# Kernel optimization log

Hardware: AMD Instinct MI355X
Metric: run time of the kernel (lower is better)

The kernel has to match this reference:

```python
import jax, jax.numpy as jnp
import numpy as np

B, C, N, D, K, M, E, G = 2, 64, 16384, 3, 128, 1, 262144, 3


def setup_inputs() -> dict:
    key = jax.random.key(0)
    ks = jax.random.split(key, 15)
    scale = 1.0 / (C * C)
    return {
        "x": jax.random.normal(ks[0], (B, C, N), jnp.float32),
        "nodes": jax.random.uniform(ks[1], (B, N, D), jnp.float32),
        "node_weights": jax.random.uniform(ks[2], (B, N, M), jnp.float32),
        "geo": jax.random.normal(ks[3], (B, G, N), jnp.float32),
        "directed_edges": jax.random.randint(ks[4], (B, E, 2), 0, N, jnp.int32),
        "edge_gradient_weights": 0.1 * jax.random.normal(ks[5], (B, E, D), jnp.float32),
        "modes": jax.random.normal(ks[6], (K, D, M), jnp.float32),
        "weights_c": scale * jax.random.uniform(ks[7], (C, C, K, M), jnp.float32),
        "weights_s": scale * jax.random.uniform(ks[8], (C, C, K, M), jnp.float32),
        "weights_0": scale * jax.random.uniform(ks[9], (C, C, 1, M), jnp.float32),
        "W": jax.random.normal(ks[10], (C, C), jnp.float32) / np.sqrt(C),
        "gw": jax.random.normal(ks[11], (C, C * D), jnp.float32) / np.sqrt(C * D),
        "geo_wx": jax.random.normal(ks[12], (C, G), jnp.float32) / np.sqrt(G),
        "wx": jax.random.normal(ks[13], (C, C), jnp.float32) / np.sqrt(C),
        "w2": jax.random.normal(ks[14], (C, C), jnp.float32) / np.sqrt(C),
    }


def reference(x, nodes, node_weights, geo, directed_edges, edge_gradient_weights,
              modes, weights_c, weights_s, weights_0, W, gw, geo_wx, wx, w2):
    # ---- Fourier bases: cos(kx), sin(kx), 1 -------------------------------
    temp = jnp.einsum('bxd,kdw->bxkw', nodes, modes)          # [B,N,K,M]
    bases_c, bases_s = jnp.cos(temp), jnp.sin(temp)
    b, n = temp.shape[0], temp.shape[1]
    bases_0 = jnp.ones((b, n, 1, temp.shape[3]), temp.dtype)
    nw = node_weights[:, :, None, :]                          # quadrature weights
    wb_c, wb_s, wb_0 = bases_c * nw, bases_s * nw, bases_0 * nw

    # ---- Spectral convolution (non-uniform Fourier neural layer) ----------
    x_c = jnp.einsum('bix,bxkw->bikw', x, wb_c)
    x_s = -jnp.einsum('bix,bxkw->bikw', x, wb_s)
    x_0 = jnp.einsum('bix,bxkw->bikw', x, wb_0)
    f_c = jnp.einsum('bikw,iokw->bokw', x_c, weights_c) - jnp.einsum('bikw,iokw->bokw', x_s, weights_s)
    f_s = jnp.einsum('bikw,iokw->bokw', x_s, weights_c) + jnp.einsum('bikw,iokw->bokw', x_c, weights_s)
    f_0 = jnp.einsum('bikw,iokw->bokw', x_0, weights_0)
    x1 = (jnp.einsum('bokw,bxkw->box', f_0, bases_0)
          + 2.0 * jnp.einsum('bokw,bxkw->box', f_c, bases_c)
          - 2.0 * jnp.einsum('bokw,bxkw->box', f_s, bases_s))

    # ---- Pointwise linear W ----------------------------------------------
    x2 = jnp.einsum('oi,bix->box', W, x)

    # ---- Least-squares gradient via edge gather + scatter-add -------------
    fT = jnp.transpose(x, (0, 2, 1))                          # [B,N,C]
    tgt, src = directed_edges[..., 0], directed_edges[..., 1]  # [B,E]
    f_src = jnp.take_along_axis(fT, src[:, :, None], axis=1)   # [B,E,C]
    f_tgt = jnp.take_along_axis(fT, tgt[:, :, None], axis=1)
    df = f_src - f_tgt
    # message[b,e,c,d] = w[b,e,d] * df[b,e,c], flattened c-major -> [B,E,C*D]
    msg = (df[..., :, None] * edge_gradient_weights[..., None, :]).reshape(b, tgt.shape[1], -1)
    gradf = jnp.zeros((b, n, msg.shape[-1]), msg.dtype).at[jnp.arange(b)[:, None], tgt].add(msg)
    x3 = jnp.einsum('og,bng->bon', gw, gradf)                  # [B,C,N]

    # ---- Geo embedding: w2 @ (softsign(geo_wx@geo) * (wx@x)) --------------
    h = jax.nn.soft_sign(jnp.einsum('og,bgx->box', geo_wx, geo)) * jnp.einsum('oi,bix->box', wx, x)
    x4 = jnp.einsum('oi,bix->box', w2, h)

    return jax.nn.gelu(x1 + x2 + x3 + x4, approximate=False)
```

## Files before the change

### kernel.cpp

```cpp
#include <hip/hip_runtime.h>
#include <hip/hip_fp16.h>
#include <math.h>

#define BB 2
#define CC 64
#define NN 16384
#define DD 3
#define KK 128
#define EE 262144
#define GG 3
#define PP 128
#define LL (NN/PP)
#define KTOT 576

typedef short bf16x8 __attribute__((ext_vector_type(8)));
typedef float f32x4  __attribute__((ext_vector_type(4)));

__device__ __forceinline__ short f2bf(float f) {
    unsigned u = __float_as_uint(f);
    u += 0x7FFF + ((u >> 16) & 1);
    return (short)(u >> 16);
}
__device__ __forceinline__ float bf2f(unsigned short u) {
    return __uint_as_float(((unsigned)u) << 16);
}

constexpr size_t OFF_XB   = 0;
constexpr size_t OFF_PC   = OFF_XB   + (size_t)BB*NN*32;
constexpr size_t OFF_PS   = OFF_PC   + (size_t)BB*PP*CC*KK;
constexpr size_t OFF_BIN4 = OFF_PC;
constexpr size_t OFF_AC   = OFF_PS   + (size_t)BB*PP*CC*KK;
constexpr size_t OFF_AS   = OFF_AC   + (size_t)BB*CC*KK;
constexpr size_t OFF_F0   = OFF_AS   + (size_t)BB*CC*KK;
constexpr size_t OFF_X0   = OFF_F0   + (size_t)BB*CC;
constexpr size_t OFF_CNT  = OFF_X0   + (size_t)BB*CC;
constexpr size_t OFF_OFFS = OFF_CNT  + (size_t)BB*NN;
constexpr size_t OFF_RANK = OFF_OFFS + (size_t)BB*NN;
constexpr size_t OFF_GRB  = OFF_RANK + (size_t)BB*EE;
constexpr size_t OFF_APAN = OFF_GRB  + (size_t)BB*NN*96;
constexpr size_t OFF_GWXT = OFF_APAN + (size_t)BB*KTOT*CC/2;

#define S_A0 (BB*(NN/64))
#define S_A1 (S_A0 + BB*CC)
#define S_A2 (S_A1 + (BB*EE)/256)
#define S_A3 (S_A2 + 48)
#define S_A4 (S_A3 + BB*PP*4)
__global__ void __launch_bounds__(256) k1(const float* __restrict__ x,
                                          const float* __restrict__ nwt,
                                          const int* __restrict__ edges,
                                          const float* __restrict__ W,
                                          const float* __restrict__ gw,
                                          const float* __restrict__ geo_wx,
                                          const float* __restrict__ w2,
                                          const float* __restrict__ nodes,
                                          const float* __restrict__ modes,
                                          unsigned short* __restrict__ xB,
                                          float* __restrict__ x0,
                                          int* __restrict__ counts,
                                          int* __restrict__ rank,
                                          float* __restrict__ gwxT,
                                          short* __restrict__ ApanB,
                                          float* __restrict__ pc,
                                          float* __restrict__ ps) {
    int blk = blockIdx.x;
    int tid = threadIdx.x;
    __shared__ __align__(16) char smem[36864];
    if (blk < S_A0) {
        float (*tile)[65] = (float (*)[65])smem;
        int b = blk / (NN/64);
        int n0 = (blk % (NN/64)) * 64;
        int c = tid & 63, r4 = tid >> 6;
        for (int rr = 0; rr < 16; rr++) {
            int i = r4*16 + rr;
            tile[i][c] = x[((size_t)b*CC + i)*NN + n0 + c];
        }
        __syncthreads();
        for (int rr = 0; rr < 16; rr++) {
            int nn = r4*16 + rr;
            xB[((size_t)b*NN + n0 + nn)*64 + c] = (unsigned short)f2bf(tile[c][nn]);
        }
    } else if (blk < S_A1) {
        float* red = (float*)smem;
        int bi = blk - S_A0;
        int b = bi >> 6, i = bi & 63;
        const float4* __restrict__ xr = (const float4*)&x[((size_t)b*CC + i)*NN];
        const float4* __restrict__ wr = (const float4*)&nwt[(size_t)b*NN];
        float s = 0.f;
        for (int t = tid; t < NN/4; t += 256) {
            float4 xv = xr[t];
            float4 wv = wr[t];
            s += xv.x*wv.x + xv.y*wv.y + xv.z*wv.z + xv.w*wv.w;
        }
        red[tid] = s;
        __syncthreads();
        for (int off = 128; off > 0; off >>= 1) {
            if (tid < off) red[tid] += red[tid+off];
            __syncthreads();
        }
        if (tid == 0) x0[b*CC + i] = red[0];
    } else if (blk < S_A2) {
        int idx = (blk - S_A1)*256 + tid;
        int tgt = edges[(size_t)idx*2 + 0];
        int b = idx / EE;
        rank[idx] = atomicAdd(&counts[b*NN + tgt], 1);
    } else if (blk < S_A3) {
        int idx = (blk - S_A2)*256 + tid;
        if (idx < CC*CC) {
            int j = idx>>6, o = idx&63;
            short wv  = f2bf(W[o*CC+j]);
            short w2v = f2bf(w2[o*CC+j]);
            ApanB[((size_t)(0*CC+o))*KTOT + 256 + j] = wv;
            ApanB[((size_t)(1*CC+o))*KTOT + 256 + j] = wv;
            ApanB[((size_t)(0*CC+o))*KTOT + 320 + j] = w2v;
            ApanB[((size_t)(1*CC+o))*KTOT + 320 + j] = w2v;
        }
        if (idx < CC*CC*DD) {
            int g = idx>>6, o = idx&63;
            short gv = f2bf(gw[o*(CC*DD)+g]);
            ApanB[((size_t)(0*CC+o))*KTOT + 384 + g] = gv;
            ApanB[((size_t)(1*CC+o))*KTOT + 384 + g] = gv;
        }
        if (idx < GG*CC) { int g = idx>>6, i = idx&63; gwxT[idx] = geo_wx[i*GG+g]; }
    } else {
        short* Axw = (short*)smem;
        short* Bc  = (short*)(smem + 17408);
        short* Bsn = (short*)(smem + 17408 + 8704);
        float* ndl = (float*)(smem + 17408 + 8704 + 8704);
        int bc = blk - S_A3;
        int b = bc >> 9;
        int rem = bc & 511;
        int chunk = rem >> 2;
        int kt = rem & 3;
        int k0 = kt * 32;
        int nbase = chunk * LL;
        int lane = tid & 63;
        int w = tid >> 6;
        int col = lane & 15;
        int quad = lane >> 4;
        int wk = w & 1;
        int wi = w >> 1;

        for (int e = tid; e < LL*3; e += 256) ndl[e] = nodes[((size_t)b*NN + nbase)*3 + e];
#pragma unroll
        for (int s = 0; s < 8; s++) {
            int e = tid + s*256;
            int i = e >> 5, seg = e & 31;
            float4 xv = *(const float4*)&x[((size_t)b*CC + i)*NN + nbase + seg*4];
            float4 wv = *(const float4*)&nwt[(size_t)b*NN + nbase + seg*4];
            unsigned lo = (unsigned)(unsigned short)f2bf(xv.x*wv.x)
                        | ((unsigned)(unsigned short)f2bf(xv.y*wv.y) << 16);
            unsigned hi = (unsigned)(unsigned short)f2bf(xv.z*wv.z)
                        | ((unsigned)(unsigned short)f2bf(xv.w*wv.w) << 16);
            *(uint2*)&Axw[i*136 + seg*4] = make_uint2(lo, hi);
        }
        __syncthreads();
#pragma unroll
        for (int s = 0; s < 16; s++) {
            int e = tid + s*256;
            int n = e & 127, kl = e >> 7;
            int k = k0 + kl;
            float t = ndl[n*3+0]*modes[k*3+0] + ndl[n*3+1]*modes[k*3+1]
                    + ndl[n*3+2]*modes[k*3+2];
            Bc [kl*136 + n] = f2bf(__cosf(t));
            Bsn[kl*136 + n] = f2bf(__sinf(t));
        }
        __syncthreads();

        f32x4 ac[2], as4[2];
#pragma unroll
        for (int it = 0; it < 2; it++)
#pragma unroll
            for (int r = 0; r < 4; r++) { ac[it][r] = 0.f; as4[it][r] = 0.f; }

        int rowB = (wk*16 + col)*136;
#pragma unroll
        for (int ns = 0; ns < 4; ns++) {
            int koff = ns*32 + quad*8;
            bf16x8 bcf = *(bf16x8*)&Bc [rowB + koff];
            bf16x8 bsf = *(bf16x8*)&Bsn[rowB + koff];
#pragma unroll
            for (int it = 0; it < 2; it++) {
                int itile = wi*2 + it;
                bf16x8 af = *(bf16x8*)&Axw[(itile*16 + col)*136 + koff];
                ac[it]  = __builtin_amdgcn_mfma_f32_16x16x32_bf16(af, bcf, ac[it], 0, 0, 0);
                as4[it] = __builtin_amdgcn_mfma_f32_16x16x32_bf16(af, bsf, as4[it], 0, 0, 0);
            }
        }
        int base = (b*PP + chunk)*CC;
        int kw = k0 + wk*16 + col;
#pragma unroll
        for (int it = 0; it < 2; it++) {
#pragma unroll
            for (int r = 0; r < 4; r++) {
                int i = (wi*2 + it)*16 + quad*4 + r;
                pc[(size_t)(base + i)*KK + kw] = ac[it][r];
                ps[(size_t)(base + i)*KK + kw] = as4[it][r];
            }
        }
    }
}

__global__ void __launch_bounds__(256) k2(const float* __restrict__ pc, const float* __restrict__ ps,
                                          float* __restrict__ Ac, float* __restrict__ As,
                                          const int* __restrict__ counts,
                                          int* __restrict__ offsets) {
    int blk = blockIdx.x;
    int tid = threadIdx.x;
    if (blk < 256) {
        int idx = blk*64 + (tid >> 2);
        int sub = tid & 3;
        if (idx >= BB*CC*KK) return;
        int b = idx / (CC*KK);
        int r = idx % (CC*KK);
        float sc = 0.f, ss = 0.f;
        for (int ch = sub; ch < PP; ch += 4) {
            size_t o = ((size_t)(b*PP + ch)*CC)*KK + r;
            sc += pc[o]; ss += ps[o];
        }
        sc += __shfl_xor(sc, 1); sc += __shfl_xor(sc, 2);
        ss += __shfl_xor(ss, 1); ss += __shfl_xor(ss, 2);
        if (sub == 0) { Ac[idx] = sc; As[idx] = ss; }
    } else {
        int b = blk - 256;
        __shared__ int part[256];
        int base = b*NN + tid*64;
        int s = 0;
        for (int j = 0; j < 64; j++) s += counts[base + j];
        part[tid] = s;
        __syncthreads();
        for (int off = 1; off < 256; off <<= 1) {
            int v = (tid >= off) ? part[tid - off] : 0;
            __syncthreads();
            part[tid] += v;
            __syncthreads();
        }
        int excl = part[tid] - s;
        for (int j = 0; j < 64; j++) {
            int c = counts[base + j];
            offsets[base + j] = excl;
            excl += c;
        }
    }
}

__global__ void __launch_bounds__(256) k3(const float* __restrict__ Ac, const float* __restrict__ As_,
                                          const float* __restrict__ wc, const float* __restrict__ wsw,
                                          const float* __restrict__ w0, const float* __restrict__ x0,
                                          const int* __restrict__ edges, const float* __restrict__ egw,
                                          const int* __restrict__ offs, const int* __restrict__ rank,
                                          float4* __restrict__ bin4,
                                          short* __restrict__ ApanB, float* __restrict__ f0) {
    int idx = blockIdx.x;
    int tid = threadIdx.x;
    if (idx >= BB*CC*2) {
        int e = (idx - BB*CC*2)*256 + tid;
        int b = e / EE;
        int tgt = edges[(size_t)e*2+0];
        int src = edges[(size_t)e*2+1];
        const float* __restrict__ ew = &egw[(size_t)e*3];
        float e0 = ew[0], e1 = ew[1], e2 = ew[2];
        int pos = offs[b*NN+tgt] + rank[e];
        bin4[(size_t)b*EE + pos] = make_float4(__int_as_float(src), e0, e1, e2);
        return;
    }
    int b = idx / (CC*2);
    int rem = idx % (CC*2);
    int o = rem >> 1, khalf = rem & 1;
    int kl = tid & 63, ig = tid >> 6;
    int k = khalf*64 + kl;
    float fc = 0.f, fs = 0.f;
    for (int ii = 0; ii < 16; ii++) {
        int i = ig*16 + ii;
        float a_c = Ac[(b*CC+i)*KK + k];
        float a_s = As_[(b*CC+i)*KK + k];
        float wcc = wc[((size_t)(i*CC+o))*KK + k];
        float wss = wsw[((size_t)(i*CC+o))*KK + k];
        fc += a_c*wcc + a_s*wss;
        fs += a_c*wss - a_s*wcc;
    }
    __shared__ float rc[256], rs[256];
    __shared__ float f0s[64];
    rc[tid] = fc; rs[tid] = fs;
    if (khalf == 0 && tid < 64) f0s[tid] = x0[b*CC + tid] * w0[tid*CC + o];
    __syncthreads();
    if (ig == 0) {
        fc = rc[kl] + rc[64+kl] + rc[128+kl] + rc[192+kl];
        fs = rs[kl] + rs[64+kl] + rs[128+kl] + rs[192+kl];
        unsigned pk = (unsigned)(unsigned short)f2bf(2.f*fc)
                    | ((unsigned)(unsigned short)f2bf(-2.f*fs) << 16);
        ((unsigned*)ApanB)[((size_t)(b*CC + o))*(KTOT/2) + k] = pk;
    }
    if (khalf == 0 && tid == 0) {
        float acc = 0.f;
        for (int i = 0; i < 64; i++) acc += f0s[i];
        f0[b*CC+o] = acc;
    }
}

#define ECAP 1024
__global__ void __launch_bounds__(256) k_edge(const unsigned short* __restrict__ xB,
                                              const int* __restrict__ offsets,
                                              const float4* __restrict__ bin4,
                                              unsigned short* __restrict__ gradfB) {
    int blk = blockIdx.x;
    int b = blk / (NN/16);
    int n0 = (blk % (NN/16)) * 16;
    int tid = threadIdx.x;
    int lane = tid & 63;
    int w = tid >> 6;
    __shared__ float4 ebuf[ECAP];
    __shared__ float gl[16][193];
    __shared__ int soff[17];
    if (tid < 16) soff[tid] = offsets[b*NN + n0 + tid];
    if (tid == 16) soff[16] = (n0 + 16 < NN) ? offsets[b*NN + n0 + 16] : EE;
    __syncthreads();
    int base = soff[0];
    int end  = soff[16];
    const unsigned short* __restrict__ xBb = xB + (size_t)b*NN*64 + lane;

    float a0[4], a1[4], a2[4], s0[4], s1[4], s2[4];
#pragma unroll
    for (int q = 0; q < 4; q++) { a0[q]=a1[q]=a2[q]=0.f; s0[q]=s1[q]=s2[q]=0.f; }

    for (int cs = base; cs < end; cs += ECAP) {
        int ce = min(cs + ECAP, end);
        __syncthreads();
        for (int t = cs + tid; t < ce; t += 256)
            ebuf[t - cs] = bin4[(size_t)b*EE + t];
        __syncthreads();
#pragma unroll
        for (int q = 0; q < 4; q++) {
            int nl = w*4 + q;
            int js = max(soff[nl], cs);
            int je = min(soff[nl+1], ce);
#pragma unroll 4
            for (int j = js; j < je; j++) {
                float4 e = ebuf[j - cs];
                int src = __float_as_int(e.x);
                float xs = bf2f(xBb[(size_t)src*64]);
                a0[q] = fmaf(xs, e.y, a0[q]);
                a1[q] = fmaf(xs, e.z, a1[q]);
                a2[q] = fmaf(xs, e.w, a2[q]);
                s0[q] += e.y; s1[q] += e.z; s2[q] += e.w;
            }
        }
    }
    __syncthreads();
#pragma unroll
    for (int q = 0; q < 4; q++) {
        int nl = w*4 + q;
        float xtgt = bf2f(xBb[(size_t)(n0 + nl)*64]);
        gl[nl][lane*3+0] = a0[q] - xtgt*s0[q];
        gl[nl][lane*3+1] = a1[q] - xtgt*s1[q];
        gl[nl][lane*3+2] = a2[q] - xtgt*s2[q];
    }
    __syncthreads();
    for (int t = tid; t < 16*192; t += 256) {
        int nl = t / 192, g = t % 192;
        gradfB[((size_t)(b*NN + n0 + nl))*192 + g] = (unsigned short)f2bf(gl[nl][g]);
    }
}

__global__ void __launch_bounds__(256) k_gemm(const unsigned short* __restrict__ xB,
                                              const float* __restrict__ nodes,
                                              const float* __restrict__ modes,
                                              const float* __restrict__ geo,
                                              const unsigned short* __restrict__ gradfB,
                                              const short* __restrict__ ApanB,
                                              const float* __restrict__ f0,
                                              const float* __restrict__ wx,
                                              const float* __restrict__ gwxT,
                                              float* __restrict__ out) {
    int blk = blockIdx.x;
    int b  = blk >> 8;
    int n0 = (blk & 255) * 64;
    int tid = threadIdx.x;
    int lane = tid & 63;
    int w = tid >> 6;
    int w16 = w * 16;
    int col  = lane & 15;
    int quad = lane >> 4;
    int quad8 = quad * 8;
    int quad4 = quad * 4;

    __shared__ __align__(16) short As[64*72];
    __shared__ __align__(16) short Bs[64*72];
    __shared__ __align__(16) short Ws[64*72];
    __shared__ float ndl[192];
    __shared__ float geo3[192];

    for (int e = tid; e < 4096; e += 256) {
        int i = e >> 6, j = e & 63;
        Ws[i*72 + j] = f2bf(wx[i*64 + j]);
    }
    if (tid < 192) ndl[tid]  = nodes[((size_t)b*NN + n0)*3 + tid];
    if (tid < 192) geo3[tid] = geo[((size_t)b*GG + (tid >> 6))*NN + n0 + (tid & 63)];

    f32x4 acc[4], xwa[4];
    float f0v[4];
#pragma unroll
    for (int r = 0; r < 4; r++) f0v[r] = f0[b*CC + w16 + quad4 + r];
#pragma unroll
    for (int nt = 0; nt < 4; nt++) {
#pragma unroll
        for (int r = 0; r < 4; r++) { acc[nt][r] = f0v[r]; xwa[nt][r] = 0.f; }
    }

    const short* __restrict__ Ab = ApanB + ((size_t)b*CC)*KTOT;

    for (int c = 0; c < 9; c++) {
        __syncthreads();
        for (int e = tid; e < 512; e += 256) {
            int o = e >> 3, seg = e & 7;
            *(uint4*)&As[o*72 + seg*8] =
                *(const uint4*)&Ab[(size_t)o*KTOT + c*64 + seg*8];
        }
        if (c < 4) {
#pragma unroll
            for (int s = 0; s < 8; s++) {
                int e = tid + s*256;
                int n = e >> 5, kpl = e & 31;
                int kp = c*32 + kpl;
                float t = ndl[n*3+0]*modes[kp*3+0] + ndl[n*3+1]*modes[kp*3+1]
                        + ndl[n*3+2]*modes[kp*3+2];
                unsigned pk = (unsigned)(unsigned short)f2bf(__cosf(t))
                            | ((unsigned)(unsigned short)f2bf(__sinf(t)) << 16);
                ((unsigned*)Bs)[n*36 + kpl] = pk;
            }
        } else if (c == 4) {
            for (int e = tid; e < 512; e += 256) {
                int n = e >> 3, seg = e & 7;
                *(uint4*)&Bs[n*72 + seg*8] =
                    *(const uint4*)&xB[((size_t)(b*NN + n0 + n))*64 + seg*8];
            }
        } else if (c == 5) {
#pragma unroll
            for (int r = 0; r < 4; r++) {
                int i = w16 + quad4 + r;
                float g0 = gwxT[i], g1 = gwxT[64+i], g2 = gwxT[128+i];
#pragma unroll
                for (int nt = 0; nt < 4; nt++) {
                    int n = nt*16 + col;
                    float t = g0*geo3[n] + g1*geo3[64+n] + g2*geo3[128+n];
                    float ssv = t / (1.f + fabsf(t));
                    Bs[n*72 + i] = f2bf(ssv * xwa[nt][r]);
                }
            }
        } else {
            const unsigned short* __restrict__ src = gradfB + (size_t)(c-6)*64;
            for (int e = tid; e < 512; e += 256) {
                int n = e >> 3, seg = e & 7;
                *(uint4*)&Bs[n*72 + seg*8] =
                    *(const uint4*)&src[((size_t)(b*NN + n0 + n))*192 + seg*8];
            }
        }
        __syncthreads();
        int rowA = (w16 + col) * 72;
#pragma unroll
        for (int ko = 0; ko < 2; ko++) {
            int koff = ko*32 + quad8;
            bf16x8 af = *(bf16x8*)&As[rowA + koff];
            if (c == 4) {
                bf16x8 wf = *(bf16x8*)&Ws[rowA + koff];
#pragma unroll
                for (int nt = 0; nt < 4; nt++) {
                    bf16x8 bfv = *(bf16x8*)&Bs[(nt*16 + col)*72 + koff];
                    acc[nt] = __builtin_amdgcn_mfma_f32_16x16x32_bf16(af, bfv, acc[nt], 0, 0, 0);
                    xwa[nt] = __builtin_amdgcn_mfma_f32_16x16x32_bf16(wf, bfv, xwa[nt], 0, 0, 0);
                }
            } else {
#pragma unroll
                for (int nt = 0; nt < 4; nt++) {
                    bf16x8 bfv = *(bf16x8*)&Bs[(nt*16 + col)*72 + koff];
                    acc[nt] = __builtin_amdgcn_mfma_f32_16x16x32_bf16(af, bfv, acc[nt], 0, 0, 0);
                }
            }
        }
    }
#pragma unroll
    for (int nt = 0; nt < 4; nt++) {
#pragma unroll
        for (int r = 0; r < 4; r++) {
            int o = w16 + quad4 + r;
            float v = acc[nt][r];
            float g = 0.5f * v * (1.f + erff(v * 0.70710678118654752f));
            out[((size_t)b*CC + o)*NN + n0 + nt*16 + col] = g;
        }
    }
}

extern "C" void kernel_launch(void* const* d_in, const int* in_sizes, int n_in,
                              void* d_out, int out_size, void* d_ws, size_t ws_size,
                              hipStream_t stream) {
    const float* x      = (const float*)d_in[0];
    const float* nodes  = (const float*)d_in[1];
    const float* nwt    = (const float*)d_in[2];
    const float* geo    = (const float*)d_in[3];
    const int*   edges  = (const int*)d_in[4];
    const float* egw    = (const float*)d_in[5];
    const float* modes  = (const float*)d_in[6];
    const float* wc     = (const float*)d_in[7];
    const float* wsw    = (const float*)d_in[8];
    const float* w0     = (const float*)d_in[9];
    const float* W      = (const float*)d_in[10];
    const float* gw     = (const float*)d_in[11];
    const float* geo_wx = (const float*)d_in[12];
    const float* wx     = (const float*)d_in[13];
    const float* w2     = (const float*)d_in[14];

    float* ws   = (float*)d_ws;
    unsigned short* xB  = (unsigned short*)(ws + OFF_XB);
    float* pc   = ws + OFF_PC;
    float* ps   = ws + OFF_PS;
    float* Ac   = ws + OFF_AC;
    float* As_  = ws + OFF_AS;
    float* f0   = ws + OFF_F0;
    float* x0   = ws + OFF_X0;
    int*  counts = (int*)(ws + OFF_CNT);
    int*  offs   = (int*)(ws + OFF_OFFS);
    int*  rank   = (int*)(ws + OFF_RANK);
    float4* bin4 = (float4*)(ws + OFF_BIN4);
    unsigned short* gradfB = (unsigned short*)(ws + OFF_GRB);
    short* ApanB  = (short*)(ws + OFF_APAN);
    float* gwxT   = ws + OFF_GWXT;
    float* out  = (float*)d_out;

    hipMemsetAsync(counts, 0, (size_t)(BB*NN)*sizeof(int), stream);

    k1 <<<S_A4, 256, 0, stream>>>(x, nwt, edges, W, gw, geo_wx, w2, nodes, modes,
                                  xB, x0, counts, rank, gwxT, ApanB, pc, ps);
    k2 <<<256 + BB, 256, 0, stream>>>(pc, ps, Ac, As_, counts, offs);
    k3 <<<BB*CC*2 + (BB*EE)/256, 256, 0, stream>>>(Ac, As_, wc, wsw, w0, x0,
                                                   edges, egw, offs, rank, bin4, ApanB, f0);
    k_edge <<<BB*(NN/16), 256, 0, stream>>>(xB, offs, bin4, gradfB);
    k_gemm <<<BB*(NN/64), 256, 0, stream>>>(xB, nodes, modes, geo, gradfB, ApanB, f0,
                                            wx, gwxT, out);
}
```

Before: 198.3 us.

## Fuse edge-gradient gather into GEMM kernel, keeping gradf in shared memory

Merges the edge gather/accumulate kernel into the GEMM/epilogue kernel. Each 64-node block now computes its own gradient features in four 16-node passes and writes them as bf16 into shared memory, where the GEMM consumes them directly. This removes the global gradfB round-trip and one kernel launch. In exchange, the fused kernel uses about 56 KB of shared memory and launches 512 blocks instead of 2048, which lowers occupancy and parallelism in the latency-bound gather phase.

Result: slower. 208.3 us (+5.1%).

```diff
diff --git a/kernel.cpp b/kernel.cpp
--- a/kernel.cpp
+++ b/kernel.cpp
@@ -297,80 +297,18 @@
     }
 }
 
-#define ECAP 1024
-__global__ void __launch_bounds__(256) k_edge(const unsigned short* __restrict__ xB,
-                                              const int* __restrict__ offsets,
-                                              const float4* __restrict__ bin4,
-                                              unsigned short* __restrict__ gradfB) {
-    int blk = blockIdx.x;
-    int b = blk / (NN/16);
-    int n0 = (blk % (NN/16)) * 16;
-    int tid = threadIdx.x;
-    int lane = tid & 63;
-    int w = tid >> 6;
-    __shared__ float4 ebuf[ECAP];
-    __shared__ float gl[16][193];
-    __shared__ int soff[17];
-    if (tid < 16) soff[tid] = offsets[b*NN + n0 + tid];
-    if (tid == 16) soff[16] = (n0 + 16 < NN) ? offsets[b*NN + n0 + 16] : EE;
-    __syncthreads();
-    int base = soff[0];
-    int end  = soff[16];
-    const unsigned short* __restrict__ xBb = xB + (size_t)b*NN*64 + lane;
-
-    float a0[4], a1[4], a2[4], s0[4], s1[4], s2[4];
-#pragma unroll
-    for (int q = 0; q < 4; q++) { a0[q]=a1[q]=a2[q]=0.f; s0[q]=s1[q]=s2[q]=0.f; }
-
-    for (int cs = base; cs < end; cs += ECAP) {
-        int ce = min(cs + ECAP, end);
-        __syncthreads();
-        for (int t = cs + tid; t < ce; t += 256)
-            ebuf[t - cs] = bin4[(size_t)b*EE + t];
-        __syncthreads();
-#pragma unroll
-        for (int q = 0; q < 4; q++) {
-            int nl = w*4 + q;
-            int js = max(soff[nl], cs);
-            int je = min(soff[nl+1], ce);
-#pragma unroll 4
-            for (int j = js; j < je; j++) {
-                float4 e = ebuf[j - cs];
-                int src = __float_as_int(e.x);
-                float xs = bf2f(xBb[(size_t)src*64]);
-                a0[q] = fmaf(xs, e.y, a0[q]);
-                a1[q] = fmaf(xs, e.z, a1[q]);
-                a2[q] = fmaf(xs, e.w, a2[q]);
-                s0[q] += e.y; s1[q] += e.z; s2[q] += e.w;
-            }
-        }
-    }
-    __syncthreads();
-#pragma unroll
-    for (int q = 0; q < 4; q++) {
-        int nl = w*4 + q;
-        float xtgt = bf2f(xBb[(size_t)(n0 + nl)*64]);
-        gl[nl][lane*3+0] = a0[q] - xtgt*s0[q];
-        gl[nl][lane*3+1] = a1[q] - xtgt*s1[q];
-        gl[nl][lane*3+2] = a2[q] - xtgt*s2[q];
-    }
-    __syncthreads();
-    for (int t = tid; t < 16*192; t += 256) {
-        int nl = t / 192, g = t % 192;
-        gradfB[((size_t)(b*NN + n0 + nl))*192 + g] = (unsigned short)f2bf(gl[nl][g]);
-    }
-}
-
-__global__ void __launch_bounds__(256) k_gemm(const unsigned short* __restrict__ xB,
-                                              const float* __restrict__ nodes,
-                                              const float* __restrict__ modes,
-                                              const float* __restrict__ geo,
-                                              const unsigned short* __restrict__ gradfB,
-                                              const short* __restrict__ ApanB,
-                                              const float* __restrict__ f0,
-                                              const float* __restrict__ wx,
-                                              const float* __restrict__ gwxT,
-                                              float* __restrict__ out) {
+#define ECAP2 512
+__global__ void __launch_bounds__(256) k_eg(const unsigned short* __restrict__ xB,
+                                            const int* __restrict__ offsets,
+                                            const float4* __restrict__ bin4,
+                                            const float* __restrict__ nodes,
+                                            const float* __restrict__ modes,
+                                            const float* __restrict__ geo,
+                                            const short* __restrict__ ApanB,
+                                            const float* __restrict__ f0,
+                                            const float* __restrict__ wx,
+                                            const float* __restrict__ gwxT,
+                                            float* __restrict__ out) {
     int blk = blockIdx.x;
     int b  = blk >> 8;
     int n0 = (blk & 255) * 64;
@@ -383,19 +321,73 @@
     int quad8 = quad * 8;
     int quad4 = quad * 4;
 
-    __shared__ __align__(16) short As[64*72];
-    __shared__ __align__(16) short Bs[64*72];
-    __shared__ __align__(16) short Ws[64*72];
-    __shared__ float ndl[192];
-    __shared__ float geo3[192];
+    __shared__ __align__(16) char smem[56832];
+    short* As = (short*)smem;
+    short* Bs = (short*)(smem + 9216);
+    short* Ws = (short*)(smem + 18432);
+    float4* ebuf = (float4*)smem;
+    int* soff = (int*)(smem + 8192);
+    unsigned short* gradfL = (unsigned short*)(smem + 27648);
+    float* ndl  = (float*)(smem + 55296);
+    float* geo3 = (float*)(smem + 56064);
+
+    if (tid < 192) ndl[tid]  = nodes[((size_t)b*NN + n0)*3 + tid];
+    if (tid < 192) geo3[tid] = geo[((size_t)b*GG + (tid >> 6))*NN + n0 + (tid & 63)];
+    if (tid < 65)  soff[tid] = (n0 + tid < NN) ? offsets[b*NN + n0 + tid] : EE;
+    __syncthreads();
+
+    const unsigned short* __restrict__ xBb = xB + (size_t)b*NN*64 + lane;
+    for (int r = 0; r < 4; r++) {
+        int nb = r*16;
+        int base = soff[nb];
+        int end  = soff[nb+16];
+        float a0[4], a1[4], a2[4], s0[4], s1[4], s2[4];
+#pragma unroll
+        for (int q = 0; q < 4; q++) { a0[q]=a1[q]=a2[q]=0.f; s0[q]=s1[q]=s2[q]=0.f; }
+        for (int cs = base; cs < end; cs += ECAP2) {
+            int ce = min(cs + ECAP2, end);
+            __syncthreads();
+            for (int t = cs + tid; t < ce; t += 256)
+                ebuf[t - cs] = bin4[(size_t)b*EE + t];
+            __syncthreads();
+#pragma unroll
+            for (int q = 0; q < 4; q++) {
+                int nl = nb + w*4 + q;
+                int js = max(soff[nl], cs);
+                int je = min(soff[nl+1], ce);
+#pragma unroll 4
+                for (int j = js; j < je; j++) {
+                    float4 e = ebuf[j - cs];
+                    int src = __float_as_int(e.x);
+                    float xs = bf2f(xBb[(size_t)src*64]);
+                    a0[q] = fmaf(xs, e.y, a0[q]);
+                    a1[q] = fmaf(xs, e.z, a1[q]);
+                    a2[q] = fmaf(xs, e.w, a2[q]);
+                    s0[q] += e.y; s1[q] += e.z; s2[q] += e.w;
+                }
+            }
+        }
+#pragma unroll
+        for (int q = 0; q < 4; q++) {
+            int nl = nb + w*4 + q;
+            float xtgt = bf2f(xBb[(size_t)(n0 + nl)*64]);
+            float fv0 = a0[q] - xtgt*s0[q];
+            float fv1 = a1[q] - xtgt*s1[q];
+            float fv2 = a2[q] - xtgt*s2[q];
+            int g0 = lane*3;
+            gradfL[(g0>>6)*4608 + nl*72 + (g0&63)] = (unsigned short)f2bf(fv0);
+            int g1 = g0+1;
+            gradfL[(g1>>6)*4608 + nl*72 + (g1&63)] = (unsigned short)f2bf(fv1);
+            int g2 = g0+2;
+            gradfL[(g2>>6)*4608 + nl*72 + (g2&63)] = (unsigned short)f2bf(fv2);
+        }
+    }
+    __syncthreads();
 
     for (int e = tid; e < 4096; e += 256) {
         int i = e >> 6, j = e & 63;
         Ws[i*72 + j] = f2bf(wx[i*64 + j]);
     }
-    if (tid < 192) ndl[tid]  = nodes[((size_t)b*NN + n0)*3 + tid];
-    if (tid < 192) geo3[tid] = geo[((size_t)b*GG + (tid >> 6))*NN + n0 + (tid & 63)];
-
     f32x4 acc[4], xwa[4];
     float f0v[4];
 #pragma unroll
@@ -446,15 +438,9 @@
                     Bs[n*72 + i] = f2bf(ssv * xwa[nt][r]);
                 }
             }
-        } else {
-            const unsigned short* __restrict__ src = gradfB + (size_t)(c-6)*64;
-            for (int e = tid; e < 512; e += 256) {
-                int n = e >> 3, seg = e & 7;
-                *(uint4*)&Bs[n*72 + seg*8] =
-                    *(const uint4*)&src[((size_t)(b*NN + n0 + n))*192 + seg*8];
-            }
-        }
-        __syncthreads();
+        }
+        __syncthreads();
+        const short* Bbase = (c >= 6) ? (const short*)&gradfL[(size_t)(c-6)*4608] : Bs;
         int rowA = (w16 + col) * 72;
 #pragma unroll
         for (int ko = 0; ko < 2; ko++) {
@@ -464,14 +450,14 @@
                 bf16x8 wf = *(bf16x8*)&Ws[rowA + koff];
 #pragma unroll
                 for (int nt = 0; nt < 4; nt++) {
-                    bf16x8 bfv = *(bf16x8*)&Bs[(nt*16 + col)*72 + koff];
+                    bf16x8 bfv = *(bf16x8*)&Bbase[(nt*16 + col)*72 + koff];
                     acc[nt] = __builtin_amdgcn_mfma_f32_16x16x32_bf16(af, bfv, acc[nt], 0, 0, 0);
                     xwa[nt] = __builtin_amdgcn_mfma_f32_16x16x32_bf16(wf, bfv, xwa[nt], 0, 0, 0);
                 }
             } else {
 #pragma unroll
                 for (int nt = 0; nt < 4; nt++) {
-                    bf16x8 bfv = *(bf16x8*)&Bs[(nt*16 + col)*72 + koff];
+                    bf16x8 bfv = *(bf16x8*)&Bbase[(nt*16 + col)*72 + koff];
                     acc[nt] = __builtin_amdgcn_mfma_f32_16x16x32_bf16(af, bfv, acc[nt], 0, 0, 0);
                 }
             }
@@ -520,7 +506,6 @@
     int*  offs   = (int*)(ws + OFF_OFFS);
     int*  rank   = (int*)(ws + OFF_RANK);
     float4* bin4 = (float4*)(ws + OFF_BIN4);
-    unsigned short* gradfB = (unsigned short*)(ws + OFF_GRB);
     short* ApanB  = (short*)(ws + OFF_APAN);
     float* gwxT   = ws + OFF_GWXT;
     float* out  = (float*)d_out;
@@ -532,7 +517,6 @@
     k2 <<<256 + BB, 256, 0, stream>>>(pc, ps, Ac, As_, counts, offs);
     k3 <<<BB*CC*2 + (BB*EE)/256, 256, 0, stream>>>(Ac, As_, wc, wsw, w0, x0,
                                                    edges, egw, offs, rank, bin4, ApanB, f0);
-    k_edge <<<BB*(NN/16), 256, 0, stream>>>(xB, offs, bin4, gradfB);
-    k_gemm <<<BB*(NN/64), 256, 0, stream>>>(xB, nodes, modes, geo, gradfB, ApanB, f0,
-                                            wx, gwxT, out);
-}
+    k_eg <<<BB*(NN/64), 256, 0, stream>>>(xB, offs, bin4, nodes, modes, geo,
+                                          ApanB, f0, wx, gwxT, out);
+}
```
